# Kernel optimization log

Hardware: AMD Instinct MI355X
Metric: run time of the kernel (lower is better)

Reference implementation:

```python
import jax, jax.numpy as jnp
import numpy as np

N_NODES = 50000

def _sage_conv(x, src, dst, W_l, b_l, W_r):
    # mean aggregation of source features onto destination nodes
    gathered = jnp.take(x, src, axis=0)                      # [E, d]
    summed = jax.ops.segment_sum(gathered, dst, num_segments=N_NODES)  # [N, d]
    deg = jax.ops.segment_sum(jnp.ones_like(dst, dtype=x.dtype), dst, num_segments=N_NODES)
    mean_nb = summed / jnp.maximum(deg, 1.0)[:, None]
    # PyG SAGEConv: lin_l(aggregated) + lin_r(self), bias on lin_l only
    return mean_nb @ W_l + b_l + x @ W_r


def setup_inputs() -> dict:
    key = jax.random.key(0)
    ks = jax.random.split(key, 8)
    d = 256
    E = 800000
    s = 1.0 / np.sqrt(d)
    x = jax.random.normal(ks[0], (N_NODES, d), dtype=jnp.float32)
    ei = jax.random.randint(ks[1], (2, E), 0, N_NODES, dtype=jnp.int64)
    W1_l = jax.random.normal(ks[2], (d, d), dtype=jnp.float32) * s
    b1 = jnp.zeros((d,), dtype=jnp.float32)
    W1_r = jax.random.normal(ks[3], (d, d), dtype=jnp.float32) * s
    W2_l = jax.random.normal(ks[4], (d, d), dtype=jnp.float32) * s
    b2 = jnp.zeros((d,), dtype=jnp.float32)
    W2_r = jax.random.normal(ks[5], (d, d), dtype=jnp.float32) * s
    return {"x": x, "ei": ei, "W1_l": W1_l, "b1": b1, "W1_r": W1_r,
            "W2_l": W2_l, "b2": b2, "W2_r": W2_r}


def reference(x, ei, W1_l, b1, W1_r, W2_l, b2, W2_r):
    src, dst = ei[0], ei[1]
    h = jax.nn.relu(_sage_conv(x, src, dst, W1_l, b1, W1_r))
    # dropout is identity in eval mode (training=False)
    h = _sage_conv(h, src, dst, W2_l, b2, W2_r)
    return h
```

## Files before the change

kernel.cpp:

```cpp
#include <hip/hip_runtime.h>
#include <hip/hip_bf16.h>
#include <cstdint>
#include <cstddef>

typedef __attribute__((ext_vector_type(8))) short s16x8;
typedef __attribute__((ext_vector_type(4))) float f32x4;

#define CAP 64

static __device__ __forceinline__ float u2f(unsigned int u) {
    union { unsigned int i; float f; } c; c.i = u; return c.f;
}
static __device__ __forceinline__ unsigned short f2b(float f) {
    union { float f; unsigned int i; } c; c.f = f;
    unsigned int x = c.i;
    x += 0x7fffu + ((x >> 16) & 1u);
    return (unsigned short)(x >> 16);
}

static __device__ __forceinline__ void acc8(float* acc, const int4& t) {
    acc[0] += u2f(((unsigned)t.x) << 16);
    acc[1] += u2f(((unsigned)t.x) & 0xffff0000u);
    acc[2] += u2f(((unsigned)t.y) << 16);
    acc[3] += u2f(((unsigned)t.y) & 0xffff0000u);
    acc[4] += u2f(((unsigned)t.z) << 16);
    acc[5] += u2f(((unsigned)t.z) & 0xffff0000u);
    acc[6] += u2f(((unsigned)t.w) << 16);
    acc[7] += u2f(((unsigned)t.w) & 0xffff0000u);
}

__global__ void build_kernel(const int* __restrict__ src, const int* __restrict__ dst,
                             int E, int* __restrict__ cnt, int* __restrict__ colp) {
    const int base = blockIdx.x * 1024 + threadIdx.x;
    int d[4], s[4];
    bool ok[4];
#pragma unroll
    for (int k = 0; k < 4; k++) {
        const int i = base + k * 256;
        ok[k] = (i < E);
        d[k] = ok[k] ? dst[i] : 0;
        s[k] = ok[k] ? src[i] : 0;
    }
    int p[4];
#pragma unroll
    for (int k = 0; k < 4; k++)
        if (ok[k]) p[k] = atomicAdd(&cnt[d[k]], 1);
#pragma unroll
    for (int k = 0; k < 4; k++)
        if (ok[k] && p[k] < CAP) colp[d[k] * CAP + p[k]] = s[k];
}

__global__ __launch_bounds__(256) void prep_kernel(const float* __restrict__ x,
                                                   unsigned short* __restrict__ xb, int n4, int nbc,
                                                   const float* __restrict__ W1l, const float* __restrict__ W1r,
                                                   unsigned short* __restrict__ Bt1,
                                                   const float* __restrict__ W2l, const float* __restrict__ W2r,
                                                   unsigned short* __restrict__ Bt2) {
    const int b = blockIdx.x;
    if (b < nbc) {
        const int i = b * 256 + threadIdx.x;
        if (i < n4) {
            float4 v = *(const float4*)(x + (size_t)i * 4);
            ushort4 o;
            o.x = f2b(v.x); o.y = f2b(v.y); o.z = f2b(v.z); o.w = f2b(v.w);
            *(ushort4*)(xb + (size_t)i * 4) = o;
        }
    } else {
        const int job = b - nbc;
        const int idx = (job & 511) * 256 + threadIdx.x;
        const float* Wl = (job < 512) ? W1l : W2l;
        const float* Wr = (job < 512) ? W1r : W2r;
        unsigned short* Bt = (job < 512) ? Bt1 : Bt2;
        const int n = idx >> 9;
        const int k = idx & 511;
        float v = (k < 256) ? Wl[(size_t)k * 256 + n] : Wr[(size_t)(k - 256) * 256 + n];
        Bt[idx] = f2b(v);
    }
}

__global__ __launch_bounds__(512) void aggregate_kernel(const unsigned short* __restrict__ xb,
                                                        const int* __restrict__ cnt,
                                                        const int* __restrict__ colp,
                                                        unsigned short* __restrict__ mean,
                                                        int N) {
    const int n = blockIdx.x * 8 + (threadIdx.x >> 6);
    if (n >= N) return;
    const int lane = threadIdx.x & 63;
    const int h = lane >> 5;
    const int l31 = lane & 31;
    const int degT = cnt[n];
    const int degS = degT < CAP ? degT : CAP;

    int idx = 0;
    if (lane < degS) idx = colp[n * CAP + lane];
    const unsigned short* basep = xb + l31 * 8;

    float acc[8];
#pragma unroll
    for (int k = 0; k < 8; k++) acc[k] = 0.f;

    const bool big = (degS > 16);

    int4 v[16];
#pragma unroll
    for (int u = 0; u < 8; u++) {
        const int e = 2 * u + h;
        const int cidx = __shfl(idx, e);
        if (e < degS) v[u] = *(const int4*)(basep + (size_t)cidx * 256);
        else          v[u] = int4{0, 0, 0, 0};
    }
    if (big) {
#pragma unroll
        for (int u = 8; u < 16; u++) {
            const int e = 2 * u + h;
            const int cidx = __shfl(idx, e);
            if (e < degS) v[u] = *(const int4*)(basep + (size_t)cidx * 256);
            else          v[u] = int4{0, 0, 0, 0};
        }
    }
#pragma unroll
    for (int u = 0; u < 8; u++) acc8(acc, v[u]);
    if (big) {
#pragma unroll
        for (int u = 8; u < 16; u++) acc8(acc, v[u]);
    }

#pragma unroll 1
    for (int base = 32; base < degS; base += 16) {
        int4 w[8];
#pragma unroll
        for (int u = 0; u < 8; u++) {
            const int e = base + 2 * u + h;
            const int cidx = __shfl(idx, e);
            if (e < degS) w[u] = *(const int4*)(basep + (size_t)cidx * 256);
            else          w[u] = int4{0, 0, 0, 0};
        }
#pragma unroll
        for (int u = 0; u < 8; u++) acc8(acc, w[u]);
    }

#pragma unroll
    for (int k = 0; k < 8; k++) acc[k] += __shfl_xor(acc[k], 32);

    if (h == 0) {
        const float inv = 1.0f / (float)(degT > 0 ? degT : 1);
        union { unsigned short us[8]; int4 v; } o;
#pragma unroll
        for (int k = 0; k < 8; k++) o.us[k] = f2b(acc[k] * inv);
        *(int4*)(mean + (size_t)n * 256 + l31 * 8) = o.v;
    }
}

template <int RELU>
__global__ __launch_bounds__(256) void gemm_kernel(const unsigned short* __restrict__ A0,
                                                   const unsigned short* __restrict__ A1,
                                                   const unsigned short* __restrict__ Bt,
                                                   const float* __restrict__ bias,
                                                   float* __restrict__ outF,
                                                   unsigned short* __restrict__ outB,
                                                   int M) {
    __shared__ unsigned short smem[6][128 * 32];
    const int tid = threadIdx.x;
    const int m0 = blockIdx.x * 128;
    const int n0 = blockIdx.y * 128;
    const int wave = tid >> 6, lane = tid & 63;
    const int wm = (wave >> 1) * 64, wn = (wave & 1) * 64;
    const int lr = lane & 15, lg = lane >> 4;
    const int srow = tid >> 2;
    const int sseg = tid & 3;

    int gm0 = m0 + srow;       if (gm0 >= M) gm0 = M - 1;
    int gm1 = m0 + srow + 64;  if (gm1 >= M) gm1 = M - 1;

    const int ldsb = wave * 1024;
    const int gseg = sseg ^ ((srow >> 1) & 3);

    f32x4 acc[4][4];
#pragma unroll
    for (int i = 0; i < 4; i++)
#pragma unroll
        for (int j = 0; j < 4; j++) acc[i][j] = (f32x4)0.0f;

    auto stage = [&](int buf, int kt) {
        const int k0 = kt * 32;
        const unsigned short* Asrc = (k0 < 256) ? A0 : A1;
        const int kk = k0 & 255;
        char* asb = (char*)(&smem[buf][0]);
        char* bsb = (char*)(&smem[3 + buf][0]);
        __builtin_amdgcn_global_load_lds(
            (const __attribute__((address_space(1))) void*)(Asrc + (size_t)gm0 * 256 + kk + gseg * 8),
            (__attribute__((address_space(3))) void*)(asb + ldsb), 16, 0, 0);
        __builtin_amdgcn_global_load_lds(
            (const __attribute__((address_space(1))) void*)(Asrc + (size_t)gm1 * 256 + kk + gseg * 8),
            (__attribute__((address_space(3))) void*)(asb + 4096 + ldsb), 16, 0, 0);
        __builtin_amdgcn_global_load_lds(
            (const __attribute__((address_space(1))) void*)(Bt + (size_t)(n0 + srow) * 512 + k0 + gseg * 8),
            (__attribute__((address_space(3))) void*)(bsb + ldsb), 16, 0, 0);
        __builtin_amdgcn_global_load_lds(
            (const __attribute__((address_space(1))) void*)(Bt + (size_t)(n0 + srow + 64) * 512 + k0 + gseg * 8),
            (__attribute__((address_space(3))) void*)(bsb + 4096 + ldsb), 16, 0, 0);
    };

    stage(0, 0);
    stage(1, 1);
    stage(2, 2);

    int cur = 0;
#pragma unroll 1
    for (int kt = 0; kt < 16; kt++) {
        if (kt <= 13)      asm volatile("s_waitcnt vmcnt(8)" ::: "memory");
        else if (kt == 14) asm volatile("s_waitcnt vmcnt(4)" ::: "memory");
        else               asm volatile("s_waitcnt vmcnt(0)" ::: "memory");
        __builtin_amdgcn_s_barrier();
        asm volatile("" ::: "memory");
        __builtin_amdgcn_sched_barrier(0);

        s16x8 a[4], b[4];
#pragma unroll
        for (int i = 0; i < 4; i++) {
            const int row = wm + i * 16 + lr;
            const int seg = lg ^ ((row >> 1) & 3);
            a[i] = *(const s16x8*)(&smem[cur][row * 32 + seg * 8]);
        }
#pragma unroll
        for (int j = 0; j < 4; j++) {
            const int row = wn + j * 16 + lr;
            const int seg = lg ^ ((row >> 1) & 3);
            b[j] = *(const s16x8*)(&smem[3 + cur][row * 32 + seg * 8]);
        }
#pragma unroll
        for (int i = 0; i < 4; i++)
#pragma unroll
            for (int j = 0; j < 4; j++)
                acc[i][j] = __builtin_amdgcn_mfma_f32_16x16x32_bf16(a[i], b[j], acc[i][j], 0, 0, 0);

        asm volatile("s_waitcnt lgkmcnt(0)" ::: "memory");
        __builtin_amdgcn_sched_barrier(0);
        __builtin_amdgcn_s_barrier();
        asm volatile("" ::: "memory");
        __builtin_amdgcn_sched_barrier(0);

        if (kt < 13) stage(cur, kt + 3);
        cur = (cur == 2) ? 0 : cur + 1;
    }

    float* wbase = ((float*)&smem[0][0]) + wave * 2304;
#pragma unroll
    for (int hf = 0; hf < 2; hf++) {
#pragma unroll
        for (int j2 = 0; j2 < 2; j2++) {
            const int j = hf * 2 + j2;
            const int n = n0 + wn + j * 16 + lr;
            const float bv = bias[n];
#pragma unroll
            for (int i = 0; i < 4; i++)
#pragma unroll
                for (int r = 0; r < 4; r++) {
                    const int row = i * 16 + lg * 4 + r;
                    float v = acc[i][j][r] + bv;
                    if (RELU) v = fmaxf(v, 0.0f);
                    wbase[row * 36 + j2 * 16 + lr] = v;
                }
        }
        asm volatile("s_waitcnt lgkmcnt(0)" ::: "memory");
        __builtin_amdgcn_sched_barrier(0);
        if (RELU) {
#pragma unroll
            for (int c = 0; c < 4; c++) {
                const int row = (lane >> 2) + 16 * c;
                const int col8 = (lane & 3) * 8;
                const int gm = m0 + wm + row;
                f32x4 t0 = *(f32x4*)(wbase + row * 36 + col8);
                f32x4 t1 = *(f32x4*)(wbase + row * 36 + col8 + 4);
                union { unsigned short us[8]; int4 v; } o;
#pragma unroll
                for (int q = 0; q < 4; q++) { o.us[q] = f2b(t0[q]); o.us[4 + q] = f2b(t1[q]); }
                if (gm < M)
                    *(int4*)(outB + (size_t)gm * 256 + n0 + wn + hf * 32 + col8) = o.v;
            }
        } else {
#pragma unroll
            for (int c = 0; c < 8; c++) {
                const int row = (lane >> 3) + 8 * c;
                const int col4 = (lane & 7) * 4;
                const int gm = m0 + wm + row;
                f32x4 t = *(f32x4*)(wbase + row * 36 + col4);
                if (gm < M)
                    *(f32x4*)(outF + (size_t)gm * 256 + n0 + wn + hf * 32 + col4) = t;
            }
        }
        asm volatile("s_waitcnt lgkmcnt(0)" ::: "memory");
        __builtin_amdgcn_sched_barrier(0);
    }
}

extern "C" void kernel_launch(void* const* d_in, const int* in_sizes, int n_in,
                              void* d_out, int out_size, void* d_ws, size_t ws_size,
                              hipStream_t stream) {
    const float* x   = (const float*)d_in[0];
    const int*   ei  = (const int*)d_in[1];
    const float* W1l = (const float*)d_in[2];
    const float* b1  = (const float*)d_in[3];
    const float* W1r = (const float*)d_in[4];
    const float* W2l = (const float*)d_in[5];
    const float* b2  = (const float*)d_in[6];
    const float* W2r = (const float*)d_in[7];
    float* out = (float*)d_out;

    const int N = in_sizes[0] / 256;
    const int E = in_sizes[1] / 2;
    const int* src = ei;
    const int* dst = ei + E;

    char* ws = (char*)d_ws;
    size_t off = 0;
    auto alloc = [&](size_t bytes) -> void* {
        void* p = ws + off;
        off += (bytes + 255) & ~(size_t)255;
        return p;
    };
    int* cnt  = (int*)alloc((size_t)N * 4);
    int* colp = (int*)alloc((size_t)N * CAP * 4);
    unsigned short* xb  = (unsigned short*)alloc((size_t)N * 256 * 2);
    unsigned short* hb  = (unsigned short*)alloc((size_t)N * 256 * 2);
    unsigned short* mb  = (unsigned short*)alloc((size_t)N * 256 * 2);
    unsigned short* Bt1 = (unsigned short*)alloc((size_t)256 * 512 * 2);
    unsigned short* Bt2 = (unsigned short*)alloc((size_t)256 * 512 * 2);

    hipMemsetAsync(cnt, 0, (size_t)N * 4, stream);
    build_kernel<<<(E + 1023) / 1024, 256, 0, stream>>>(src, dst, E, cnt, colp);

    const int n4 = N * 256 / 4;
    const int nbc = (n4 + 255) / 256;
    prep_kernel<<<nbc + 1024, 256, 0, stream>>>(x, xb, n4, nbc, W1l, W1r, Bt1, W2l, W2r, Bt2);

    const int mtiles = (N + 127) / 128;
    dim3 ggrid(mtiles, 2);
    const int ablocks = (N + 7) / 8;

    aggregate_kernel<<<ablocks, 512, 0, stream>>>(xb, cnt, colp, mb, N);
    gemm_kernel<1><<<ggrid, 256, 0, stream>>>(mb, xb, Bt1, b1, nullptr, hb, N);

    aggregate_kernel<<<ablocks, 512, 0, stream>>>(hb, cnt, colp, mb, N);
    gemm_kernel<0><<<ggrid, 256, 0, stream>>>(mb, hb, Bt2, b2, out, nullptr, N);
}
```

Before: 322.9 us.

## Use BK=64 double-buffered GEMM with setprio and fold count memset into prep

The GEMM k-tile grows from 32 to 64, with two LDS buffers instead of three and a new XOR swizzle over 8 segments. The next stage's loads are now issued before the MFMA block, which runs at raised wave priority, so the loop has half as many barriers and better load/compute overlap. The hipMemsetAsync of the degree counters is replaced by extra blocks in the prep kernel, removing one launch. Pipeline depth drops from three stages to two, which may expose more memory latency.

```diff
diff --git a/kernel.cpp b/kernel.cpp
--- a/kernel.cpp
+++ b/kernel.cpp
@@ -55,7 +55,8 @@
                                                    const float* __restrict__ W1l, const float* __restrict__ W1r,
                                                    unsigned short* __restrict__ Bt1,
                                                    const float* __restrict__ W2l, const float* __restrict__ W2r,
-                                                   unsigned short* __restrict__ Bt2) {
+                                                   unsigned short* __restrict__ Bt2,
+                                                   int* __restrict__ cnt, int N) {
     const int b = blockIdx.x;
     if (b < nbc) {
         const int i = b * 256 + threadIdx.x;
@@ -65,7 +66,7 @@
             o.x = f2b(v.x); o.y = f2b(v.y); o.z = f2b(v.z); o.w = f2b(v.w);
             *(ushort4*)(xb + (size_t)i * 4) = o;
         }
-    } else {
+    } else if (b < nbc + 1024) {
         const int job = b - nbc;
         const int idx = (job & 511) * 256 + threadIdx.x;
         const float* Wl = (job < 512) ? W1l : W2l;
@@ -75,6 +76,9 @@
         const int k = idx & 511;
         float v = (k < 256) ? Wl[(size_t)k * 256 + n] : Wr[(size_t)(k - 256) * 256 + n];
         Bt[idx] = f2b(v);
+    } else {
+        const int i = (b - nbc - 1024) * 256 + threadIdx.x;
+        if (i < N) cnt[i] = 0;
     }
 }
 
@@ -159,21 +163,23 @@
                                                    float* __restrict__ outF,
                                                    unsigned short* __restrict__ outB,
                                                    int M) {
-    __shared__ unsigned short smem[6][128 * 32];
+    __shared__ unsigned short smem[4][128 * 64];
     const int tid = threadIdx.x;
     const int m0 = blockIdx.x * 128;
     const int n0 = blockIdx.y * 128;
     const int wave = tid >> 6, lane = tid & 63;
     const int wm = (wave >> 1) * 64, wn = (wave & 1) * 64;
     const int lr = lane & 15, lg = lane >> 4;
-    const int srow = tid >> 2;
-    const int sseg = tid & 3;
-
-    int gm0 = m0 + srow;       if (gm0 >= M) gm0 = M - 1;
-    int gm1 = m0 + srow + 64;  if (gm1 >= M) gm1 = M - 1;
-
-    const int ldsb = wave * 1024;
-    const int gseg = sseg ^ ((srow >> 1) & 3);
+
+    const int r8 = lane >> 3;
+    const int koffs = ((lane & 7) ^ r8) * 8;
+    int arow[4], brow[4];
+#pragma unroll
+    for (int q = 0; q < 4; q++) {
+        int r = m0 + (wave * 4 + q) * 8 + r8;
+        arow[q] = (r < M) ? r : (M - 1);
+        brow[q] = n0 + (wave * 4 + q) * 8 + r8;
+    }
 
     f32x4 acc[4][4];
 #pragma unroll
@@ -182,57 +188,52 @@
         for (int j = 0; j < 4; j++) acc[i][j] = (f32x4)0.0f;
 
     auto stage = [&](int buf, int kt) {
-        const int k0 = kt * 32;
+        const int k0 = kt * 64;
         const unsigned short* Asrc = (k0 < 256) ? A0 : A1;
         const int kk = k0 & 255;
         char* asb = (char*)(&smem[buf][0]);
-        char* bsb = (char*)(&smem[3 + buf][0]);
-        __builtin_amdgcn_global_load_lds(
-            (const __attribute__((address_space(1))) void*)(Asrc + (size_t)gm0 * 256 + kk + gseg * 8),
-            (__attribute__((address_space(3))) void*)(asb + ldsb), 16, 0, 0);
-        __builtin_amdgcn_global_load_lds(
-            (const __attribute__((address_space(1))) void*)(Asrc + (size_t)gm1 * 256 + kk + gseg * 8),
-            (__attribute__((address_space(3))) void*)(asb + 4096 + ldsb), 16, 0, 0);
-        __builtin_amdgcn_global_load_lds(
-            (const __attribute__((address_space(1))) void*)(Bt + (size_t)(n0 + srow) * 512 + k0 + gseg * 8),
-            (__attribute__((address_space(3))) void*)(bsb + ldsb), 16, 0, 0);
-        __builtin_amdgcn_global_load_lds(
-            (const __attribute__((address_space(1))) void*)(Bt + (size_t)(n0 + srow + 64) * 512 + k0 + gseg * 8),
-            (__attribute__((address_space(3))) void*)(bsb + 4096 + ldsb), 16, 0, 0);
+        char* bsb = (char*)(&smem[2 + buf][0]);
+#pragma unroll
+        for (int q = 0; q < 4; q++)
+            __builtin_amdgcn_global_load_lds(
+                (const __attribute__((address_space(1))) void*)(Asrc + (size_t)arow[q] * 256 + kk + koffs),
+                (__attribute__((address_space(3))) void*)(asb + (wave * 4 + q) * 1024), 16, 0, 0);
+#pragma unroll
+        for (int q = 0; q < 4; q++)
+            __builtin_amdgcn_global_load_lds(
+                (const __attribute__((address_space(1))) void*)(Bt + (size_t)brow[q] * 512 + k0 + koffs),
+                (__attribute__((address_space(3))) void*)(bsb + (wave * 4 + q) * 1024), 16, 0, 0);
     };
 
     stage(0, 0);
     stage(1, 1);
-    stage(2, 2);
-
-    int cur = 0;
+
 #pragma unroll 1
-    for (int kt = 0; kt < 16; kt++) {
-        if (kt <= 13)      asm volatile("s_waitcnt vmcnt(8)" ::: "memory");
-        else if (kt == 14) asm volatile("s_waitcnt vmcnt(4)" ::: "memory");
-        else               asm volatile("s_waitcnt vmcnt(0)" ::: "memory");
+    for (int t = 0; t < 8; t++) {
+        if (t < 7) asm volatile("s_waitcnt vmcnt(8)" ::: "memory");
+        else       asm volatile("s_waitcnt vmcnt(0)" ::: "memory");
         __builtin_amdgcn_s_barrier();
         asm volatile("" ::: "memory");
         __builtin_amdgcn_sched_barrier(0);
 
-        s16x8 a[4], b[4];
-#pragma unroll
-        for (int i = 0; i < 4; i++) {
-            const int row = wm + i * 16 + lr;
-            const int seg = lg ^ ((row >> 1) & 3);
-            a[i] = *(const s16x8*)(&smem[cur][row * 32 + seg * 8]);
-        }
-#pragma unroll
-        for (int j = 0; j < 4; j++) {
-            const int row = wn + j * 16 + lr;
-            const int seg = lg ^ ((row >> 1) & 3);
-            b[j] = *(const s16x8*)(&smem[3 + cur][row * 32 + seg * 8]);
-        }
-#pragma unroll
-        for (int i = 0; i < 4; i++)
-#pragma unroll
-            for (int j = 0; j < 4; j++)
-                acc[i][j] = __builtin_amdgcn_mfma_f32_16x16x32_bf16(a[i], b[j], acc[i][j], 0, 0, 0);
+        const int cur = t & 1;
+        s16x8 a[2][4], b[2][4];
+#pragma unroll
+        for (int ks = 0; ks < 2; ks++)
+#pragma unroll
+            for (int i = 0; i < 4; i++) {
+                const int row = wm + i * 16 + lr;
+                const int u = (ks * 4 + lg) ^ (lr & 7);
+                a[ks][i] = *(const s16x8*)(&smem[cur][row * 64 + u * 8]);
+            }
+#pragma unroll
+        for (int ks = 0; ks < 2; ks++)
+#pragma unroll
+            for (int j = 0; j < 4; j++) {
+                const int row = wn + j * 16 + lr;
+                const int u = (ks * 4 + lg) ^ (lr & 7);
+                b[ks][j] = *(const s16x8*)(&smem[2 + cur][row * 64 + u * 8]);
+            }
 
         asm volatile("s_waitcnt lgkmcnt(0)" ::: "memory");
         __builtin_amdgcn_sched_barrier(0);
@@ -240,8 +241,17 @@
         asm volatile("" ::: "memory");
         __builtin_amdgcn_sched_barrier(0);
 
-        if (kt < 13) stage(cur, kt + 3);
-        cur = (cur == 2) ? 0 : cur + 1;
+        if (t < 6) stage(cur, t + 2);
+
+        __builtin_amdgcn_s_setprio(1);
+#pragma unroll
+        for (int ks = 0; ks < 2; ks++)
+#pragma unroll
+            for (int i = 0; i < 4; i++)
+#pragma unroll
+                for (int j = 0; j < 4; j++)
+                    acc[i][j] = __builtin_amdgcn_mfma_f32_16x16x32_bf16(a[ks][i], b[ks][j], acc[i][j], 0, 0, 0);
+        __builtin_amdgcn_s_setprio(0);
     }
 
     float* wbase = ((float*)&smem[0][0]) + wave * 2304;
@@ -327,12 +337,13 @@
     unsigned short* Bt1 = (unsigned short*)alloc((size_t)256 * 512 * 2);
     unsigned short* Bt2 = (unsigned short*)alloc((size_t)256 * 512 * 2);
 
-    hipMemsetAsync(cnt, 0, (size_t)N * 4, stream);
-    build_kernel<<<(E + 1023) / 1024, 256, 0, stream>>>(src, dst, E, cnt, colp);
-
     const int n4 = N * 256 / 4;
     const int nbc = (n4 + 255) / 256;
-    prep_kernel<<<nbc + 1024, 256, 0, stream>>>(x, xb, n4, nbc, W1l, W1r, Bt1, W2l, W2r, Bt2);
+    const int nzb = (N + 255) / 256;
+    prep_kernel<<<nbc + 1024 + nzb, 256, 0, stream>>>(x, xb, n4, nbc,
+                                                      W1l, W1r, Bt1, W2l, W2r, Bt2, cnt, N);
+
+    build_kernel<<<(E + 1023) / 1024, 256, 0, stream>>>(src, dst, E, cnt, colp);
 
     const int mtiles = (N + 127) / 128;
     dim3 ggrid(mtiles, 2);
```

Result: no change. 321.2 us (-0.5%).
